# Performance work log

Hardware: AMD Instinct MI355X
Metric: run time of the kernel (lower is better)

The kernel has to match this reference:

```python
import jax, jax.numpy as jnp
import numpy as np

LN_EPS = 1e-5

def _layernorm(x, g, b):
    mu = jnp.mean(x, axis=-1, keepdims=True)
    var = jnp.var(x, axis=-1, keepdims=True)
    return (x - mu) * jax.lax.rsqrt(var + LN_EPS) * g + b

def setup_inputs() -> dict:
    key = jax.random.key(0)
    ks = jax.random.split(key, 8)
    B, T, V, H = 32, 128, 204, 128
    s = 0.02
    x = jax.random.normal(ks[0], (B, T, V, 1), dtype=jnp.float32)
    return {
        "x": x,
        # batched per-variable GRN params
        "fc1_w": jax.random.normal(ks[1], (V, H), dtype=jnp.float32) * s,
        "fc1_b": jnp.zeros((V, H), jnp.float32),
        "fc2_w": jax.random.normal(ks[2], (V, H, H), dtype=jnp.float32) * s,
        "fc2_b": jnp.zeros((V, H), jnp.float32),
        "glu_w": jax.random.normal(ks[3], (V, 2 * H, H), dtype=jnp.float32) * s,
        "glu_b": jnp.zeros((V, 2 * H), jnp.float32),
        "skip_w": jax.random.normal(ks[4], (V, H), dtype=jnp.float32) * s,
        "skip_b": jnp.zeros((V, H), jnp.float32),
        "ln_g": jnp.ones((H,), jnp.float32),
        "ln_b": jnp.zeros((H,), jnp.float32),
        # weight GRN params (input_dim=V, hidden=H, output_dim=V; identity skip)
        "wfc1_w": jax.random.normal(ks[5], (V, H), dtype=jnp.float32) * s,
        "wfc1_b": jnp.zeros((H,), jnp.float32),
        "wfc2_w": jax.random.normal(ks[6], (H, H), dtype=jnp.float32) * s,
        "wfc2_b": jnp.zeros((H,), jnp.float32),
        "wglu_w": jax.random.normal(ks[7], (H, 2 * V), dtype=jnp.float32) * s,
        "wglu_b": jnp.zeros((2 * V,), jnp.float32),
        "wln_g": jnp.ones((V,), jnp.float32),
        "wln_b": jnp.zeros((V,), jnp.float32),
    }

def reference(x, fc1_w, fc1_b, fc2_w, fc2_b, glu_w, glu_b, skip_w, skip_b, ln_g, ln_b,
              wfc1_w, wfc1_b, wfc2_w, wfc2_b, wglu_w, wglu_b, wln_g, wln_b):
    B, T, V, D = x.shape
    H = fc1_w.shape[1]
    xs = x.reshape(B * T, V)  # (N, V) since D == 1

    # --- batched per-variable GRN (eval mode: dropout is identity) ---
    h = jax.nn.elu(xs[..., None] * fc1_w + fc1_b)              # (N, V, H)
    h = jnp.einsum('nvh,vhk->nvk', h, fc2_w) + fc2_b           # bmm over V
    glu = jnp.einsum('nvh,vgh->nvg', h, glu_w) + glu_b         # (N, V, 2H)
    fc_out, gate = glu[..., :H], glu[..., H:]
    h = fc_out * jax.nn.sigmoid(gate)
    skip = xs[..., None] * skip_w + skip_b                     # (N, V, H)
    var_out = _layernorm(skip + h, ln_g, ln_b)                 # (N, V, H)

    # --- weight GRN (input_dim = output_dim = V -> identity skip) ---
    a = jax.nn.elu(xs @ wfc1_w + wfc1_b)                       # (N, H)
    a = a @ wfc2_w + wfc2_b
    g = a @ wglu_w + wglu_b                                    # (N, 2V)
    hg = g[:, :V] * jax.nn.sigmoid(g[:, V:])
    wts = jax.nn.softmax(_layernorm(xs + hg, wln_g, wln_b), axis=-1)  # (N, V)

    out = jnp.einsum('nvh,nv->nh', var_out, wts)               # (N, H)
    return out.reshape(B, T, H), wts.reshape(B, T, V)
```

## Files before the change

### kernel.cpp

```cpp
#include <hip/hip_runtime.h>
#include <hip/hip_bf16.h>

#define NROWS 4096
#define NV    204
#define NH    128
#define NG    256

#define HALF_BYTES 16384
#define SMS_OFF    (2 * HALF_BYTES)
#define SMS_BYTES  3584
#define LN_OFF     (SMS_OFF + 2 * SMS_BYTES)
#define LDS_BYTES  (LN_OFF + 1024)

typedef __bf16 bf16x8 __attribute__((ext_vector_type(8)));
typedef float  f32x4  __attribute__((ext_vector_type(4)));

__device__ __forceinline__ float elu_f(float x)  { return x > 0.f ? x : __expf(x) - 1.f; }
__device__ __forceinline__ float sigm_f(float x) { return 1.f / (1.f + __expf(-x)); }

__device__ __forceinline__ void stage16(const void* g, void* l) {
    __builtin_amdgcn_global_load_lds((const __attribute__((address_space(1))) void*)g,
                                     (__attribute__((address_space(3))) void*)l, 16, 0, 0);
}

__device__ __forceinline__ void stage_half(const void* src, char* dst, int w, int l) {
    const char* sb = (const char*)src;
    #pragma unroll
    for (int s = 0; s < 4; ++s)
        stage16(sb + (w * 4 + s) * 1024 + l * 16, dst + (w * 4 + s) * 1024);
}

__device__ __forceinline__ void stage_smalls(const float* src, char* dst, int w, int l) {
    if (w < 3)       stage16((const char*)src + w * 1024 + l * 16, dst + w * 1024);
    else if (l < 32) stage16((const char*)src + 3072 + l * 16,     dst + 3072);
}

#define NB_FC2 NV
#define NB_GLU (NV * 16)
#define NB_SM  NV
#define NB_WTS (NROWS / 8)

__global__ __launch_bounds__(256) void k_setup(
    const float* __restrict__ fc2_w, __bf16* __restrict__ fc2t,
    const float* __restrict__ glu_w, __bf16* __restrict__ glu16,
    const float* __restrict__ fc1_w, const float* __restrict__ fc1_b,
    const float* __restrict__ fc2_b, const float* __restrict__ glu_b,
    const float* __restrict__ skip_w, const float* __restrict__ skip_b,
    float* __restrict__ smalls,
    const float* __restrict__ xs,
    const float* __restrict__ wfc1_w, const float* __restrict__ wfc1_b,
    const float* __restrict__ wfc2_w, const float* __restrict__ wfc2_b,
    const float* __restrict__ wglu_w, const float* __restrict__ wglu_b,
    const float* __restrict__ wln_g,  const float* __restrict__ wln_b,
    float* __restrict__ wts)
{
    __shared__ float tile[64 * 129];
    __shared__ float sx[8][NV];
    __shared__ float sa[8][NH];
    __shared__ float sg[8][2 * NV];

    const int b = blockIdx.x;
    const int t = threadIdx.x;

    if (b < NB_FC2) {
        const int v = b;
        const float* s = fc2_w + (size_t)v * (NH * NH);
        __bf16*      d = fc2t + (size_t)v * (NH * NH);
        for (int h = 0; h < 2; ++h) {
            __syncthreads();
            for (int i = t; i < 64 * 32; i += 256) {
                const int k = i >> 5, n4 = (i & 31) * 4;
                const float4 f = *(const float4*)(s + (h * 64 + k) * 128 + n4);
                tile[k * 129 + n4 + 0] = f.x;
                tile[k * 129 + n4 + 1] = f.y;
                tile[k * 129 + n4 + 2] = f.z;
                tile[k * 129 + n4 + 3] = f.w;
            }
            __syncthreads();
            for (int i = t; i < 128 * 8; i += 256) {
                const int n = i >> 3, kc = (i & 7) * 8;
                bf16x8 o;
                #pragma unroll
                for (int q = 0; q < 8; ++q) o[q] = (__bf16)tile[(kc + q) * 129 + n];
                const int ch  = h * 8 + (i & 7);
                const int chs = ch ^ (n & 7);
                *(bf16x8*)(d + n * 128 + chs * 8) = o;
            }
        }
        return;
    }

    if (b < NB_FC2 + NB_GLU) {
        const int idx = (b - NB_FC2) * 256 + t;
        const int ch = idx & 15;
        const int g  = (idx >> 4) & 255;
        const int v  = idx >> 12;
        const float* sp = glu_w + (((size_t)v * NG + g) * NH + ch * 8);
        bf16x8 o;
        #pragma unroll
        for (int q = 0; q < 8; ++q) o[q] = (__bf16)sp[q];
        const int dch = ch ^ (g & 7);
        *(bf16x8*)(glu16 + (((size_t)v * NG + g) * NH) + dch * 8) = o;
        return;
    }

    if (b < NB_FC2 + NB_GLU + NB_SM) {
        const int v = b - (NB_FC2 + NB_GLU);
        float* dst = smalls + (size_t)v * 1024;
        for (int idx = t; idx < 896; idx += 256) {
            float val;
            if      (idx < 128)  val = fc1_w[v * NH + idx];
            else if (idx < 256)  val = fc1_b[v * NH + idx - 128];
            else if (idx < 384)  val = fc2_b[v * NH + idx - 256];
            else if (idx < 640)  val = glu_b[v * NG + idx - 384];
            else if (idx < 768)  val = skip_w[v * NH + idx - 640];
            else                 val = skip_b[v * NH + idx - 768];
            dst[idx] = val;
        }
        return;
    }

    const int r0 = (b - NB_FC2 - NB_GLU - NB_SM) * 8;
    const int tr = t >> 5;
    const int tc = t & 31;

    for (int i = t; i < 8 * NV; i += 256) {
        const int r = i / NV, c = i - r * NV;
        sx[r][c] = xs[(size_t)(r0 + r) * NV + c];
    }
    __syncthreads();

    float acc1[4];
    #pragma unroll
    for (int j = 0; j < 4; ++j) acc1[j] = wfc1_b[tc + 32 * j];
    for (int v = 0; v < NV; ++v) {
        const float xv = sx[tr][v];
        #pragma unroll
        for (int j = 0; j < 4; ++j)
            acc1[j] = fmaf(xv, wfc1_w[v * NH + tc + 32 * j], acc1[j]);
    }
    #pragma unroll
    for (int j = 0; j < 4; ++j) sa[tr][tc + 32 * j] = elu_f(acc1[j]);
    __syncthreads();

    float acc2[4];
    #pragma unroll
    for (int j = 0; j < 4; ++j) acc2[j] = wfc2_b[tc + 32 * j];
    for (int h = 0; h < NH; ++h) {
        const float av = sa[tr][h];
        #pragma unroll
        for (int j = 0; j < 4; ++j)
            acc2[j] = fmaf(av, wfc2_w[h * NH + tc + 32 * j], acc2[j]);
    }
    __syncthreads();
    #pragma unroll
    for (int j = 0; j < 4; ++j) sa[tr][tc + 32 * j] = acc2[j];
    __syncthreads();

    float accg[13];
    #pragma unroll
    for (int gi = 0; gi < 12; ++gi) accg[gi] = wglu_b[tc + 32 * gi];
    accg[12] = (tc < 24) ? wglu_b[tc + 384] : 0.f;
    for (int h = 0; h < NH; ++h) {
        const float av = sa[tr][h];
        #pragma unroll
        for (int gi = 0; gi < 12; ++gi)
            accg[gi] = fmaf(av, wglu_w[h * (2 * NV) + tc + 32 * gi], accg[gi]);
        if (tc < 24) accg[12] = fmaf(av, wglu_w[h * (2 * NV) + tc + 384], accg[12]);
    }
    __syncthreads();
    #pragma unroll
    for (int gi = 0; gi < 12; ++gi) sg[tr][tc + 32 * gi] = accg[gi];
    if (tc < 24) sg[tr][tc + 384] = accg[12];
    __syncthreads();

    float tv[7];
    float s1 = 0.f, s2 = 0.f;
    #pragma unroll
    for (int ii = 0; ii < 7; ++ii) {
        const int c = tc + 32 * ii;
        float val = 0.f;
        if (c < NV) {
            const float hg = sg[tr][c] * sigm_f(sg[tr][c + NV]);
            val = sx[tr][c] + hg;
            s1 += val; s2 = fmaf(val, val, s2);
        }
        tv[ii] = val;
    }
    #pragma unroll
    for (int m = 1; m <= 16; m <<= 1) { s1 += __shfl_xor(s1, m); s2 += __shfl_xor(s2, m); }
    const float mu  = s1 * (1.f / 204.f);
    const float var = s2 * (1.f / 204.f) - mu * mu;
    const float rs  = rsqrtf(fmaxf(var, 0.f) + 1e-5f);

    float mx = -1e30f;
    #pragma unroll
    for (int ii = 0; ii < 7; ++ii) {
        const int c = tc + 32 * ii;
        if (c < NV) {
            const float y = fmaf((tv[ii] - mu) * rs, wln_g[c], wln_b[c]);
            tv[ii] = y;
            mx = fmaxf(mx, y);
        }
    }
    #pragma unroll
    for (int m = 1; m <= 16; m <<= 1) mx = fmaxf(mx, __shfl_xor(mx, m));
    float se = 0.f;
    #pragma unroll
    for (int ii = 0; ii < 7; ++ii) {
        const int c = tc + 32 * ii;
        if (c < NV) {
            const float e = __expf(tv[ii] - mx);
            tv[ii] = e;
            se += e;
        }
    }
    #pragma unroll
    for (int m = 1; m <= 16; m <<= 1) se += __shfl_xor(se, m);
    const float inv = 1.f / se;
    #pragma unroll
    for (int ii = 0; ii < 7; ++ii) {
        const int c = tc + 32 * ii;
        if (c < NV) wts[(size_t)(r0 + tr) * NV + c] = tv[ii] * inv;
    }
}

__global__ __launch_bounds__(256, 2) void k_main(
    const float*  __restrict__ xs,
    const __bf16* __restrict__ fc2t,
    const __bf16* __restrict__ glu16,
    const float*  __restrict__ smalls,
    const float*  __restrict__ ln_g,
    const float*  __restrict__ ln_b,
    const float*  __restrict__ wts,
    float*        __restrict__ out)
{
    __shared__ __align__(16) char lds[LDS_BYTES];

    const int tid = threadIdx.x;
    const int w   = tid >> 6;
    const int l   = tid & 63;
    const int l15 = l & 15;
    const int lg  = l >> 4;
    const int sw7 = l15 & 7;

    const int vg = blockIdx.x & 7;
    const int m0 = (blockIdx.x >> 3) * 64 + w * 16;
    const int nv = (NV - 1 - vg) / 8 + 1;
    const size_t rowoff = (size_t)(m0 + l15) * NV;

    const f32x4 zero4 = {0.f, 0.f, 0.f, 0.f};
    f32x4 acc_out[8];
    #pragma unroll
    for (int j = 0; j < 8; ++j) acc_out[j] = zero4;

    const int  sh0 = l15 + ((lg & 1) << 5);
    const int  sh1 = sh0 + 16;
    const bool rlo = (lg < 2);

    const float* lnS = (const float*)(lds + LN_OFF);

    float xv, wv, xn, wn;
    {
        stage_half(fc2t + (size_t)vg * (NH * NH), lds, w, l);
        stage_smalls(smalls + (size_t)vg * 1024, lds + SMS_OFF, w, l);
        if (w == 0) {
            const char* p = (l < 32) ? ((const char*)ln_g + l * 16)
                                     : ((const char*)ln_b + (l - 32) * 16);
            stage16(p, lds + LN_OFF);
        }
        xv = xs[rowoff + vg];
        wv = wts[rowoff + vg];
    }

    for (int i = 0; i < nv; ++i) {
        const int v  = vg + 8 * i;
        const int vn = (i + 1 < nv) ? v + 8 : v;
        const float* sm = (const float*)(lds + SMS_OFF + (i & 1) * SMS_BYTES);
        const __bf16* gluv = glu16 + (size_t)v * (NG * NH);

        __syncthreads();
        stage_half(fc2t + (size_t)v * (NH * NH) + 64 * NH, lds + HALF_BYTES, w, l);

        bf16x8 a1[4];
        #pragma unroll
        for (int kb = 0; kb < 4; ++kb) {
            const int k0 = kb * 32 + lg * 8;
            const float4 w0 = *(const float4*)(sm + k0);
            const float4 w1 = *(const float4*)(sm + k0 + 4);
            const float4 b0 = *(const float4*)(sm + 128 + k0);
            const float4 b1 = *(const float4*)(sm + 128 + k0 + 4);
            bf16x8 af;
            af[0] = (__bf16)elu_f(fmaf(xv, w0.x, b0.x));
            af[1] = (__bf16)elu_f(fmaf(xv, w0.y, b0.y));
            af[2] = (__bf16)elu_f(fmaf(xv, w0.z, b0.z));
            af[3] = (__bf16)elu_f(fmaf(xv, w0.w, b0.w));
            af[4] = (__bf16)elu_f(fmaf(xv, w1.x, b1.x));
            af[5] = (__bf16)elu_f(fmaf(xv, w1.y, b1.y));
            af[6] = (__bf16)elu_f(fmaf(xv, w1.z, b1.z));
            af[7] = (__bf16)elu_f(fmaf(xv, w1.w, b1.w));
            a1[kb] = af;
        }

        f32x4 h2f[8];
        #pragma unroll
        for (int j = 0; j < 4; ++j) {
            f32x4 acc = zero4;
            const char* rp = lds + (j * 16 + l15) * 256;
            #pragma unroll
            for (int kb = 0; kb < 4; ++kb) {
                const bf16x8 wf = *(const bf16x8*)(rp + (((kb * 4 + lg) ^ sw7) << 4));
                acc = __builtin_amdgcn_mfma_f32_16x16x32_bf16(wf, a1[kb], acc, 0, 0, 0);
            }
            const float4 fb = *(const float4*)(sm + 256 + j * 16 + lg * 4);
            acc[0] += fb.x; acc[1] += fb.y; acc[2] += fb.z; acc[3] += fb.w;
            h2f[j] = acc;
        }

        __syncthreads();
        stage_half(gluv, lds, w, l);

        #pragma unroll
        for (int j = 4; j < 8; ++j) {
            f32x4 acc = zero4;
            const char* rp = lds + HALF_BYTES + ((j - 4) * 16 + l15) * 256;
            #pragma unroll
            for (int kb = 0; kb < 4; ++kb) {
                const bf16x8 wf = *(const bf16x8*)(rp + (((kb * 4 + lg) ^ sw7) << 4));
                acc = __builtin_amdgcn_mfma_f32_16x16x32_bf16(wf, a1[kb], acc, 0, 0, 0);
            }
            const float4 fb = *(const float4*)(sm + 256 + j * 16 + lg * 4);
            acc[0] += fb.x; acc[1] += fb.y; acc[2] += fb.z; acc[3] += fb.w;
            h2f[j] = acc;
        }

        bf16x8 b2[4];
        #pragma unroll
        for (int kb2 = 0; kb2 < 4; ++kb2) {
            union U { __bf16 h[4]; int i2[2]; };
            U P, Q;
            P.h[0] = (__bf16)h2f[2 * kb2 + 0][0]; P.h[1] = (__bf16)h2f[2 * kb2 + 0][1];
            P.h[2] = (__bf16)h2f[2 * kb2 + 0][2]; P.h[3] = (__bf16)h2f[2 * kb2 + 0][3];
            Q.h[0] = (__bf16)h2f[2 * kb2 + 1][0]; Q.h[1] = (__bf16)h2f[2 * kb2 + 1][1];
            Q.h[2] = (__bf16)h2f[2 * kb2 + 1][2]; Q.h[3] = (__bf16)h2f[2 * kb2 + 1][3];
            const int px0 = __shfl(P.i2[0], sh0), qx0 = __shfl(Q.i2[0], sh0);
            const int py0 = __shfl(P.i2[1], sh0), qy0 = __shfl(Q.i2[1], sh0);
            const int px1 = __shfl(P.i2[0], sh1), qx1 = __shfl(Q.i2[0], sh1);
            const int py1 = __shfl(P.i2[1], sh1), qy1 = __shfl(Q.i2[1], sh1);
            union V { int ii[4]; bf16x8 vv; } R;
            R.ii[0] = rlo ? px0 : qx0;
            R.ii[1] = rlo ? py0 : qy0;
            R.ii[2] = rlo ? px1 : qx1;
            R.ii[3] = rlo ? py1 : qy1;
            b2[kb2] = R.vv;
        }

        __syncthreads();
        stage_half(gluv + 64 * NH, lds + HALF_BYTES, w, l);

        f32x4 fco[8];
        #pragma unroll
        for (int j = 0; j < 4; ++j) {
            f32x4 acc = zero4;
            const char* rp = lds + (j * 16 + l15) * 256;
            #pragma unroll
            for (int kb = 0; kb < 4; ++kb) {
                const bf16x8 wf = *(const bf16x8*)(rp + (((kb * 4 + lg) ^ sw7) << 4));
                acc = __builtin_amdgcn_mfma_f32_16x16x32_bf16(wf, b2[kb], acc, 0, 0, 0);
            }
            const float4 gb = *(const float4*)(sm + 384 + j * 16 + lg * 4);
            acc[0] += gb.x; acc[1] += gb.y; acc[2] += gb.z; acc[3] += gb.w;
            fco[j] = acc;
        }

        __syncthreads();
        stage_half(gluv + 128 * NH, lds, w, l);

        #pragma unroll
        for (int j = 4; j < 8; ++j) {
            f32x4 acc = zero4;
            const char* rp = lds + HALF_BYTES + ((j - 4) * 16 + l15) * 256;
            #pragma unroll
            for (int kb = 0; kb < 4; ++kb) {
                const bf16x8 wf = *(const bf16x8*)(rp + (((kb * 4 + lg) ^ sw7) << 4));
                acc = __builtin_amdgcn_mfma_f32_16x16x32_bf16(wf, b2[kb], acc, 0, 0, 0);
            }
            const float4 gb = *(const float4*)(sm + 384 + j * 16 + lg * 4);
            acc[0] += gb.x; acc[1] += gb.y; acc[2] += gb.z; acc[3] += gb.w;
            fco[j] = acc;
        }

        __syncthreads();
        stage_half(gluv + 192 * NH, lds + HALF_BYTES, w, l);

        f32x4 sv[8];
        #pragma unroll
        for (int j = 0; j < 4; ++j) {
            f32x4 acc = zero4;
            const char* rp = lds + (j * 16 + l15) * 256;
            #pragma unroll
            for (int kb = 0; kb < 4; ++kb) {
                const bf16x8 wg = *(const bf16x8*)(rp + (((kb * 4 + lg) ^ sw7) << 4));
                acc = __builtin_amdgcn_mfma_f32_16x16x32_bf16(wg, b2[kb], acc, 0, 0, 0);
            }
            const float4 bga = *(const float4*)(sm + 512 + j * 16 + lg * 4);
            const float4 sw4 = *(const float4*)(sm + 640 + j * 16 + lg * 4);
            const float4 sb4 = *(const float4*)(sm + 768 + j * 16 + lg * 4);
            f32x4 s;
            s[0] = fmaf(xv, sw4.x, sb4.x) + fco[j][0] * sigm_f(acc[0] + bga.x);
            s[1] = fmaf(xv, sw4.y, sb4.y) + fco[j][1] * sigm_f(acc[1] + bga.y);
            s[2] = fmaf(xv, sw4.z, sb4.z) + fco[j][2] * sigm_f(acc[2] + bga.z);
            s[3] = fmaf(xv, sw4.w, sb4.w) + fco[j][3] * sigm_f(acc[3] + bga.w);
            sv[j] = s;
        }

        __syncthreads();
        stage_half(fc2t + (size_t)vn * (NH * NH), lds, w, l);
        stage_smalls(smalls + (size_t)vn * 1024,
                     lds + SMS_OFF + ((i + 1) & 1) * SMS_BYTES, w, l);
        xn = xs[rowoff + vn];
        wn = wts[rowoff + vn];

        #pragma unroll
        for (int j = 4; j < 8; ++j) {
            f32x4 acc = zero4;
            const char* rp = lds + HALF_BYTES + ((j - 4) * 16 + l15) * 256;
            #pragma unroll
            for (int kb = 0; kb < 4; ++kb) {
                const bf16x8 wg = *(const bf16x8*)(rp + (((kb * 4 + lg) ^ sw7) << 4));
                acc = __builtin_amdgcn_mfma_f32_16x16x32_bf16(wg, b2[kb], acc, 0, 0, 0);
            }
            const float4 bga = *(const float4*)(sm + 512 + j * 16 + lg * 4);
            const float4 sw4 = *(const float4*)(sm + 640 + j * 16 + lg * 4);
            const float4 sb4 = *(const float4*)(sm + 768 + j * 16 + lg * 4);
            f32x4 s;
            s[0] = fmaf(xv, sw4.x, sb4.x) + fco[j][0] * sigm_f(acc[0] + bga.x);
            s[1] = fmaf(xv, sw4.y, sb4.y) + fco[j][1] * sigm_f(acc[1] + bga.y);
            s[2] = fmaf(xv, sw4.z, sb4.z) + fco[j][2] * sigm_f(acc[2] + bga.z);
            s[3] = fmaf(xv, sw4.w, sb4.w) + fco[j][3] * sigm_f(acc[3] + bga.w);
            sv[j] = s;
        }

        float t1 = 0.f, t2 = 0.f;
        #pragma unroll
        for (int j = 0; j < 8; ++j) {
            #pragma unroll
            for (int r = 0; r < 4; ++r) { t1 += sv[j][r]; t2 = fmaf(sv[j][r], sv[j][r], t2); }
        }
        t1 += __shfl_xor(t1, 16); t2 += __shfl_xor(t2, 16);
        t1 += __shfl_xor(t1, 32); t2 += __shfl_xor(t2, 32);
        const float mu  = t1 * (1.f / 128.f);
        const float var = t2 * (1.f / 128.f) - mu * mu;
        const float rsv = rsqrtf(fmaxf(var, 0.f) + 1e-5f);

        #pragma unroll
        for (int j = 0; j < 8; ++j) {
            const float4 lg4 = *(const float4*)(lnS + j * 16 + lg * 4);
            const float4 lb4 = *(const float4*)(lnS + 128 + j * 16 + lg * 4);
            const float y0 = fmaf((sv[j][0] - mu) * rsv, lg4.x, lb4.x);
            const float y1 = fmaf((sv[j][1] - mu) * rsv, lg4.y, lb4.y);
            const float y2 = fmaf((sv[j][2] - mu) * rsv, lg4.z, lb4.z);
            const float y3 = fmaf((sv[j][3] - mu) * rsv, lg4.w, lb4.w);
            acc_out[j][0] = fmaf(wv, y0, acc_out[j][0]);
            acc_out[j][1] = fmaf(wv, y1, acc_out[j][1]);
            acc_out[j][2] = fmaf(wv, y2, acc_out[j][2]);
            acc_out[j][3] = fmaf(wv, y3, acc_out[j][3]);
        }

        xv = xn; wv = wn;
    }

    asm volatile("s_waitcnt vmcnt(0)" ::: "memory");

    #pragma unroll
    for (int j = 0; j < 8; ++j) {
        #pragma unroll
        for (int r = 0; r < 4; ++r)
            atomicAdd(&out[(size_t)(m0 + l15) * NH + j * 16 + lg * 4 + r], acc_out[j][r]);
    }
}

extern "C" void kernel_launch(void* const* d_in, const int* in_sizes, int n_in,
                              void* d_out, int out_size, void* d_ws, size_t ws_size,
                              hipStream_t stream) {
    (void)in_sizes; (void)n_in; (void)out_size; (void)ws_size;

    const float* xs     = (const float*)d_in[0];
    const float* fc1_w  = (const float*)d_in[1];
    const float* fc1_b  = (const float*)d_in[2];
    const float* fc2_w  = (const float*)d_in[3];
    const float* fc2_b  = (const float*)d_in[4];
    const float* glu_w  = (const float*)d_in[5];
    const float* glu_b  = (const float*)d_in[6];
    const float* skip_w = (const float*)d_in[7];
    const float* skip_b = (const float*)d_in[8];
    const float* ln_g   = (const float*)d_in[9];
    const float* ln_b   = (const float*)d_in[10];
    const float* wfc1_w = (const float*)d_in[11];
    const float* wfc1_b = (const float*)d_in[12];
    const float* wfc2_w = (const float*)d_in[13];
    const float* wfc2_b = (const float*)d_in[14];
    const float* wglu_w = (const float*)d_in[15];
    const float* wglu_b = (const float*)d_in[16];
    const float* wln_g  = (const float*)d_in[17];
    const float* wln_b  = (const float*)d_in[18];

    float* out = (float*)d_out;
    float* wts = out + (size_t)NROWS * NH;

    __bf16* fc2t   = (__bf16*)d_ws;
    __bf16* glu16  = fc2t + (size_t)NV * NH * NH;
    float*  smalls = (float*)(glu16 + (size_t)NV * NG * NH);

    hipMemsetAsync(d_out, 0, (size_t)NROWS * NH * sizeof(float), stream);

    k_setup<<<NB_FC2 + NB_GLU + NB_SM + NB_WTS, 256, 0, stream>>>(
        fc2_w, fc2t, glu_w, glu16,
        fc1_w, fc1_b, fc2_b, glu_b, skip_w, skip_b, smalls,
        xs, wfc1_w, wfc1_b, wfc2_w, wfc2_b, wglu_w, wglu_b, wln_g, wln_b, wts);

    k_main<<<(NROWS / 64) * 8, 256, 0, stream>>>(xs, fc2t, glu16, smalls,
                                                 ln_g, ln_b, wts, out);
}
```

Measured before the change: 340.0 us.

## Triple-buffer weight staging in LDS with partial vmcnt waits

Moves the staging of weight halves from a two-slot LDS ring to a three-slot ring, so each load is issued two compute phases before it is used instead of one. The __syncthreads barriers become explicit s_waitcnt vmcnt(N) plus s_barrier, which wait only for the oldest outstanding loads and not for all of them. This is meant to hide more global-to-LDS latency behind MFMA work. It costs 16KB more LDS per block, which may lower occupancy, and relies on hand-counted vmcnt values being correct.

```diff
diff --git a/kernel.cpp b/kernel.cpp
--- a/kernel.cpp
+++ b/kernel.cpp
@@ -6,8 +6,8 @@
 #define NH    128
 #define NG    256
 
-#define HALF_BYTES 16384
-#define SMS_OFF    (2 * HALF_BYTES)
+#define SLOT_B     16384
+#define SMS_OFF    (3 * SLOT_B)
 #define SMS_BYTES  3584
 #define LN_OFF     (SMS_OFF + 2 * SMS_BYTES)
 #define LDS_BYTES  (LN_OFF + 1024)
@@ -34,6 +34,12 @@
     if (w < 3)       stage16((const char*)src + w * 1024 + l * 16, dst + w * 1024);
     else if (l < 32) stage16((const char*)src + 3072 + l * 16,     dst + 3072);
 }
+
+#define PSYNC(N) do { \
+    asm volatile("s_waitcnt vmcnt(" N ")" ::: "memory"); \
+    __builtin_amdgcn_s_barrier(); \
+    asm volatile("" ::: "memory"); \
+} while (0)
 
 #define NB_FC2 NV
 #define NB_GLU (NV * 16)
@@ -249,6 +255,10 @@
     const int nv = (NV - 1 - vg) / 8 + 1;
     const size_t rowoff = (size_t)(m0 + l15) * NV;
 
+    char* const slot0 = lds;
+    char* const slot1 = lds + SLOT_B;
+    char* const slot2 = lds + 2 * SLOT_B;
+
     const f32x4 zero4 = {0.f, 0.f, 0.f, 0.f};
     f32x4 acc_out[8];
     #pragma unroll
@@ -262,13 +272,14 @@
 
     float xv, wv, xn, wn;
     {
-        stage_half(fc2t + (size_t)vg * (NH * NH), lds, w, l);
-        stage_smalls(smalls + (size_t)vg * 1024, lds + SMS_OFF, w, l);
         if (w == 0) {
             const char* p = (l < 32) ? ((const char*)ln_g + l * 16)
                                      : ((const char*)ln_b + (l - 32) * 16);
             stage16(p, lds + LN_OFF);
         }
+        stage_half(fc2t + (size_t)vg * (NH * NH), slot0, w, l);
+        stage_smalls(smalls + (size_t)vg * 1024, lds + SMS_OFF, w, l);
+        stage_half(fc2t + (size_t)vg * (NH * NH) + 64 * NH, slot1, w, l);
         xv = xs[rowoff + vg];
         wv = wts[rowoff + vg];
     }
@@ -279,8 +290,8 @@
         const float* sm = (const float*)(lds + SMS_OFF + (i & 1) * SMS_BYTES);
         const __bf16* gluv = glu16 + (size_t)v * (NG * NH);
 
-        __syncthreads();
-        stage_half(fc2t + (size_t)v * (NH * NH) + 64 * NH, lds + HALF_BYTES, w, l);
+        PSYNC("6");
+        stage_half(gluv, slot2, w, l);
 
         bf16x8 a1[4];
         #pragma unroll
@@ -306,7 +317,7 @@
         #pragma unroll
         for (int j = 0; j < 4; ++j) {
             f32x4 acc = zero4;
-            const char* rp = lds + (j * 16 + l15) * 256;
+            const char* rp = slot0 + (j * 16 + l15) * 256;
             #pragma unroll
             for (int kb = 0; kb < 4; ++kb) {
                 const bf16x8 wf = *(const bf16x8*)(rp + (((kb * 4 + lg) ^ sw7) << 4));
@@ -317,13 +328,13 @@
             h2f[j] = acc;
         }
 
-        __syncthreads();
-        stage_half(gluv, lds, w, l);
+        PSYNC("6");
+        stage_half(gluv + 64 * NH, slot0, w, l);
 
         #pragma unroll
         for (int j = 4; j < 8; ++j) {
             f32x4 acc = zero4;
-            const char* rp = lds + HALF_BYTES + ((j - 4) * 16 + l15) * 256;
+            const char* rp = slot1 + ((j - 4) * 16 + l15) * 256;
             #pragma unroll
             for (int kb = 0; kb < 4; ++kb) {
                 const bf16x8 wf = *(const bf16x8*)(rp + (((kb * 4 + lg) ^ sw7) << 4));
@@ -355,14 +366,14 @@
             b2[kb2] = R.vv;
         }
 
-        __syncthreads();
-        stage_half(gluv + 64 * NH, lds + HALF_BYTES, w, l);
+        PSYNC("4");
+        stage_half(gluv + 128 * NH, slot1, w, l);
 
         f32x4 fco[8];
         #pragma unroll
         for (int j = 0; j < 4; ++j) {
             f32x4 acc = zero4;
-            const char* rp = lds + (j * 16 + l15) * 256;
+            const char* rp = slot2 + (j * 16 + l15) * 256;
             #pragma unroll
             for (int kb = 0; kb < 4; ++kb) {
                 const bf16x8 wf = *(const bf16x8*)(rp + (((kb * 4 + lg) ^ sw7) << 4));
@@ -373,13 +384,13 @@
             fco[j] = acc;
         }
 
-        __syncthreads();
-        stage_half(gluv + 128 * NH, lds, w, l);
+        PSYNC("4");
+        stage_half(gluv + 192 * NH, slot2, w, l);
 
         #pragma unroll
         for (int j = 4; j < 8; ++j) {
             f32x4 acc = zero4;
-            const char* rp = lds + HALF_BYTES + ((j - 4) * 16 + l15) * 256;
+            const char* rp = slot0 + ((j - 4) * 16 + l15) * 256;
             #pragma unroll
             for (int kb = 0; kb < 4; ++kb) {
                 const bf16x8 wf = *(const bf16x8*)(rp + (((kb * 4 + lg) ^ sw7) << 4));
@@ -390,14 +401,14 @@
             fco[j] = acc;
         }
 
-        __syncthreads();
-        stage_half(gluv + 192 * NH, lds + HALF_BYTES, w, l);
+        PSYNC("4");
+        stage_half(fc2t + (size_t)vn * (NH * NH), slot0, w, l);
 
         f32x4 sv[8];
         #pragma unroll
         for (int j = 0; j < 4; ++j) {
             f32x4 acc = zero4;
-            const char* rp = lds + (j * 16 + l15) * 256;
+            const char* rp = slot1 + (j * 16 + l15) * 256;
             #pragma unroll
             for (int kb = 0; kb < 4; ++kb) {
                 const bf16x8 wg = *(const bf16x8*)(rp + (((kb * 4 + lg) ^ sw7) << 4));
@@ -414,17 +425,17 @@
             sv[j] = s;
         }
 
-        __syncthreads();
-        stage_half(fc2t + (size_t)vn * (NH * NH), lds, w, l);
+        PSYNC("4");
         stage_smalls(smalls + (size_t)vn * 1024,
                      lds + SMS_OFF + ((i + 1) & 1) * SMS_BYTES, w, l);
+        stage_half(fc2t + (size_t)vn * (NH * NH) + 64 * NH, slot1, w, l);
         xn = xs[rowoff + vn];
         wn = wts[rowoff + vn];
 
         #pragma unroll
         for (int j = 4; j < 8; ++j) {
             f32x4 acc = zero4;
-            const char* rp = lds + HALF_BYTES + ((j - 4) * 16 + l15) * 256;
+            const char* rp = slot2 + ((j - 4) * 16 + l15) * 256;
             #pragma unroll
             for (int kb = 0; kb < 4; ++kb) {
                 const bf16x8 wg = *(const bf16x8*)(rp + (((kb * 4 + lg) ^ sw7) << 4));
```

Measured after the change: 337.2 us. Within noise of the previous version (-0.8%).
